# Performance work log

Hardware: AMD Instinct MI355X
Metric: run time of the kernel (lower is better)

## Reference

```python
import jax, jax.numpy as jnp
import numpy as np

INPUT_SIZE = 128
HIDDEN_SIZE = 128
BATCH = 65536
K = INPUT_SIZE + HIDDEN_SIZE


def setup_inputs() -> dict:
    key = jax.random.key(0)
    ks = jax.random.split(key, 11)
    bound = 1.0 / np.sqrt(K)  # nn.Linear default init range
    inp = {
        "input": jax.random.normal(ks[0], (BATCH, INPUT_SIZE), dtype=jnp.float32),
        "hidden": jax.random.normal(ks[1], (BATCH, HIDDEN_SIZE), dtype=jnp.float32),
        "cell": jax.random.normal(ks[2], (BATCH, HIDDEN_SIZE), dtype=jnp.float32),
        # Four gate linears: weights [hidden, K], biases [hidden]
        "W_f": jax.random.uniform(ks[3], (HIDDEN_SIZE, K), jnp.float32, -bound, bound),
        "b_f": jax.random.uniform(ks[4], (HIDDEN_SIZE,), jnp.float32, -bound, bound),
        "W_i": jax.random.uniform(ks[5], (HIDDEN_SIZE, K), jnp.float32, -bound, bound),
        "b_i": jax.random.uniform(ks[6], (HIDDEN_SIZE,), jnp.float32, -bound, bound),
        "W_o": jax.random.uniform(ks[7], (HIDDEN_SIZE, K), jnp.float32, -bound, bound),
        "b_o": jax.random.uniform(ks[8], (HIDDEN_SIZE,), jnp.float32, -bound, bound),
        "W_c": jax.random.uniform(ks[9], (HIDDEN_SIZE, K), jnp.float32, -bound, bound),
        "b_c": jax.random.uniform(ks[10], (HIDDEN_SIZE,), jnp.float32, -bound, bound),
    }
    return inp


def reference(input, hidden, cell, W_f, b_f, W_i, b_i, W_o, b_o, W_c, b_c):
    # combined = cat([input, hidden], axis=1); fuse 4 gate GEMMs into one
    combined = jnp.concatenate([input, hidden], axis=1)  # [B, K]
    W = jnp.concatenate([W_f, W_i, W_o, W_c], axis=0)    # [4H, K]
    b = jnp.concatenate([b_f, b_i, b_o, b_c], axis=0)    # [4H]
    gates = combined @ W.T + b                            # [B, 4H]
    f, i, o, g = jnp.split(gates, 4, axis=1)
    forget_gate = jax.nn.sigmoid(f)
    input_gate = jax.nn.sigmoid(i)
    output_gate = jax.nn.sigmoid(o)
    cell_gate = jnp.tanh(g)
    new_cell = forget_gate * cell + input_gate * cell_gate
    new_hidden = output_gate * jnp.tanh(new_cell)
    return (new_hidden, new_cell)
```

## Files before the change

kernel.cpp:

```cpp
#include <hip/hip_runtime.h>
#include <hip/hip_bf16.h>

#define BATCH   65536
#define FEAT    128
#define KDIM    256

typedef __attribute__((ext_vector_type(8))) short bf16x8;
typedef __attribute__((ext_vector_type(4))) float f32x4;

__device__ __forceinline__ short f2bf(float f) {
    return __builtin_bit_cast(short, __float2bfloat16(f));
}

__device__ __forceinline__ bf16x8 cvt8(f32x4 lo, f32x4 hi) {
    bf16x8 r;
    r[0] = f2bf(lo[0]); r[1] = f2bf(lo[1]); r[2] = f2bf(lo[2]); r[3] = f2bf(lo[3]);
    r[4] = f2bf(hi[0]); r[5] = f2bf(hi[1]); r[6] = f2bf(hi[2]); r[7] = f2bf(hi[3]);
    return r;
}

__device__ __forceinline__ float sigmoidf_(float x) {
    return 1.0f / (1.0f + __expf(-x));
}
__device__ __forceinline__ float tanhf_(float x) {
    float xc = fminf(fmaxf(x, -15.0f), 15.0f);
    float e = __expf(-2.0f * xc);
    return (1.0f - e) / (1.0f + e);
}

__global__ __launch_bounds__(256, 4)
void lstm_ksplit(const float* __restrict__ inp, const float* __restrict__ hid,
                 const float* __restrict__ cel,
                 const float* __restrict__ Wf, const float* __restrict__ bfp,
                 const float* __restrict__ Wi, const float* __restrict__ bip,
                 const float* __restrict__ Wo, const float* __restrict__ bop,
                 const float* __restrict__ Wc, const float* __restrict__ bcp,
                 float* __restrict__ out)
{
    __shared__ float lds[4][64][35];

    const int tid  = threadIdx.x;
    const int lane = tid & 63;
    const int wid  = tid >> 6;
    const int bid  = blockIdx.x;
    const int cg   = bid >> 7;
    const int rtg  = bid & 127;

    const int lr = lane & 15;
    const int lk = lane >> 4;
    const int j  = cg * 16 + lr;

    const int kq = wid;
    const int k0 = (kq & 1) * 64;
    const float* Asrc = (kq < 2) ? inp : hid;

    bf16x8 w[4][2];
    {
        const float* wsrc[4] = {Wf, Wi, Wo, Wc};
        #pragma unroll
        for (int g = 0; g < 4; ++g) {
            const float* s = wsrc[g] + (size_t)j * KDIM + kq * 64 + lk * 8;
            #pragma unroll
            for (int ks = 0; ks < 2; ++ks) {
                f32x4 lo = *(const f32x4*)(s + ks * 32);
                f32x4 hi = *(const f32x4*)(s + ks * 32 + 4);
                w[g][ks] = cvt8(lo, hi);
            }
        }
    }
    const float bsf = bfp[j], bsi = bip[j], bso = bop[j], bsc = bcp[j];

    float* outH = out;
    float* outC = out + (size_t)BATCH * FEAT;

    for (int it = 0; it < 16; ++it) {
        const int R0 = (rtg + it * 128) * 32;

        const float* a = Asrc + (size_t)(R0 + lr) * FEAT + k0 + lk * 8;
        f32x4 alo[2][2], ahi[2][2];
        #pragma unroll
        for (int ks = 0; ks < 2; ++ks)
            #pragma unroll
            for (int mb = 0; mb < 2; ++mb) {
                alo[ks][mb] = *(const f32x4*)(a + mb * 16 * FEAT + ks * 32);
                ahi[ks][mb] = *(const f32x4*)(a + mb * 16 * FEAT + ks * 32 + 4);
            }

        f32x4 acc[2][4];
        #pragma unroll
        for (int mb = 0; mb < 2; ++mb)
            #pragma unroll
            for (int g = 0; g < 4; ++g)
                acc[mb][g] = (f32x4){0.f, 0.f, 0.f, 0.f};

        #pragma unroll
        for (int ks = 0; ks < 2; ++ks) {
            bf16x8 a0 = cvt8(alo[ks][0], ahi[ks][0]);
            bf16x8 a1 = cvt8(alo[ks][1], ahi[ks][1]);
            #pragma unroll
            for (int g = 0; g < 4; ++g) {
                acc[0][g] = __builtin_amdgcn_mfma_f32_16x16x32_bf16(a0, w[g][ks], acc[0][g], 0, 0, 0);
                acc[1][g] = __builtin_amdgcn_mfma_f32_16x16x32_bf16(a1, w[g][ks], acc[1][g], 0, 0, 0);
            }
        }

        #pragma unroll
        for (int mb = 0; mb < 2; ++mb)
            #pragma unroll
            for (int g = 0; g < 4; ++g)
                #pragma unroll
                for (int t = 0; t < 4; ++t)
                    lds[kq][lane][mb * 16 + g * 4 + t] = acc[mb][g][t];
        __syncthreads();

        #pragma unroll
        for (int p = 0; p < 2; ++p) {
            const int rl  = wid * 8 + p * 4 + (lane >> 4);
            const int jc  = lane & 15;
            const int mb  = rl >> 4;
            const int lk2 = (rl >> 2) & 3;
            const int t   = rl & 3;
            const int sl  = lk2 * 16 + jc;

            float s0 = 0.f, s1 = 0.f, s2 = 0.f, s3 = 0.f;
            #pragma unroll
            for (int q = 0; q < 4; ++q) {
                s0 += lds[q][sl][mb * 16 + 0 * 4 + t];
                s1 += lds[q][sl][mb * 16 + 1 * 4 + t];
                s2 += lds[q][sl][mb * 16 + 2 * 4 + t];
                s3 += lds[q][sl][mb * 16 + 3 * 4 + t];
            }

            const int R = R0 + rl;
            const size_t off = (size_t)R * FEAT + cg * 16 + jc;
            float cv = cel[off];
            float fg = sigmoidf_(s0 + bsf);
            float ig = sigmoidf_(s1 + bsi);
            float og = sigmoidf_(s2 + bso);
            float gg = tanhf_(s3 + bsc);
            float nc = fg * cv + ig * gg;
            float nh = og * tanhf_(nc);
            outH[off] = nh;
            outC[off] = nc;
        }
        __syncthreads();
    }
}

extern "C" void kernel_launch(void* const* d_in, const int* in_sizes, int n_in,
                              void* d_out, int out_size, void* d_ws, size_t ws_size,
                              hipStream_t stream) {
    const float* inp = (const float*)d_in[0];
    const float* hid = (const float*)d_in[1];
    const float* cel = (const float*)d_in[2];
    const float* Wf  = (const float*)d_in[3];
    const float* bf  = (const float*)d_in[4];
    const float* Wi  = (const float*)d_in[5];
    const float* bi  = (const float*)d_in[6];
    const float* Wo  = (const float*)d_in[7];
    const float* bo  = (const float*)d_in[8];
    const float* Wc  = (const float*)d_in[9];
    const float* bc  = (const float*)d_in[10];
    float* out = (float*)d_out;

    lstm_ksplit<<<dim3(1024), dim3(256), 0, stream>>>(
        inp, hid, cel, Wf, bf, Wi, bi, Wo, bo, Wc, bc, out);
}
```

Before: 213.5 us.

## Prefetch next tile's activations and cell, double-buffer packed bf16 partial sums

Loads the next iteration's A-operand rows and cell values into registers before the current tile's reduction and epilogue, so global-load latency overlaps with compute. The LDS partial-sum buffer is double-buffered, which removes the second barrier per iteration. Partial sums are packed as bf16 pairs, halving LDS traffic and footprint. This lowers precision of the k-split reduction and raises register pressure.

```diff
diff --git a/kernel.cpp b/kernel.cpp
--- a/kernel.cpp
+++ b/kernel.cpp
@@ -19,6 +19,18 @@
     return r;
 }
 
+__device__ __forceinline__ unsigned int pk2(float a, float b) {
+    unsigned short ua = __builtin_bit_cast(unsigned short, __float2bfloat16(a));
+    unsigned short ub = __builtin_bit_cast(unsigned short, __float2bfloat16(b));
+    return (unsigned int)ua | ((unsigned int)ub << 16);
+}
+__device__ __forceinline__ float bflo(unsigned int p) {
+    return __builtin_bit_cast(float, p << 16);
+}
+__device__ __forceinline__ float bfhi(unsigned int p) {
+    return __builtin_bit_cast(float, p & 0xffff0000u);
+}
+
 __device__ __forceinline__ float sigmoidf_(float x) {
     return 1.0f / (1.0f + __expf(-x));
 }
@@ -29,15 +41,15 @@
 }
 
 __global__ __launch_bounds__(256, 4)
-void lstm_ksplit(const float* __restrict__ inp, const float* __restrict__ hid,
-                 const float* __restrict__ cel,
-                 const float* __restrict__ Wf, const float* __restrict__ bfp,
-                 const float* __restrict__ Wi, const float* __restrict__ bip,
-                 const float* __restrict__ Wo, const float* __restrict__ bop,
-                 const float* __restrict__ Wc, const float* __restrict__ bcp,
-                 float* __restrict__ out)
+void lstm_v3(const float* __restrict__ inp, const float* __restrict__ hid,
+             const float* __restrict__ cel,
+             const float* __restrict__ Wf, const float* __restrict__ bfp,
+             const float* __restrict__ Wi, const float* __restrict__ bip,
+             const float* __restrict__ Wo, const float* __restrict__ bop,
+             const float* __restrict__ Wc, const float* __restrict__ bcp,
+             float* __restrict__ out)
 {
-    __shared__ float lds[4][64][35];
+    __shared__ unsigned int plds[2][4][64][17];
 
     const int tid  = threadIdx.x;
     const int lane = tid & 63;
@@ -73,11 +85,9 @@
     float* outH = out;
     float* outC = out + (size_t)BATCH * FEAT;
 
-    for (int it = 0; it < 16; ++it) {
-        const int R0 = (rtg + it * 128) * 32;
-
-        const float* a = Asrc + (size_t)(R0 + lr) * FEAT + k0 + lk * 8;
-        f32x4 alo[2][2], ahi[2][2];
+    f32x4 alo[2][2], ahi[2][2];
+    {
+        const float* a = Asrc + (size_t)((rtg * 32) + lr) * FEAT + k0 + lk * 8;
         #pragma unroll
         for (int ks = 0; ks < 2; ++ks)
             #pragma unroll
@@ -85,6 +95,16 @@
                 alo[ks][mb] = *(const f32x4*)(a + mb * 16 * FEAT + ks * 32);
                 ahi[ks][mb] = *(const f32x4*)(a + mb * 16 * FEAT + ks * 32 + 4);
             }
+    }
+    float cv[2];
+    #pragma unroll
+    for (int p = 0; p < 2; ++p) {
+        const int rl = wid * 8 + p * 4 + lk;
+        cv[p] = cel[(size_t)(rtg * 32 + rl) * FEAT + j];
+    }
+
+    for (int it = 0; it < 16; ++it) {
+        const int R0 = (rtg + it * 128) * 32;
 
         f32x4 acc[2][4];
         #pragma unroll
@@ -104,19 +124,34 @@
             }
         }
 
-        #pragma unroll
-        for (int mb = 0; mb < 2; ++mb)
-            #pragma unroll
-            for (int g = 0; g < 4; ++g)
+        if (it < 15) {
+            const int R0n = (rtg + (it + 1) * 128) * 32;
+            const float* an = Asrc + (size_t)(R0n + lr) * FEAT + k0 + lk * 8;
+            #pragma unroll
+            for (int ks = 0; ks < 2; ++ks)
                 #pragma unroll
-                for (int t = 0; t < 4; ++t)
-                    lds[kq][lane][mb * 16 + g * 4 + t] = acc[mb][g][t];
+                for (int mb = 0; mb < 2; ++mb) {
+                    alo[ks][mb] = *(const f32x4*)(an + mb * 16 * FEAT + ks * 32);
+                    ahi[ks][mb] = *(const f32x4*)(an + mb * 16 * FEAT + ks * 32 + 4);
+                }
+        }
+
+        {
+            unsigned int* dst = &plds[it & 1][kq][lane][0];
+            #pragma unroll
+            for (int mb = 0; mb < 2; ++mb)
+                #pragma unroll
+                for (int t = 0; t < 4; ++t) {
+                    dst[mb * 8 + t * 2 + 0] = pk2(acc[mb][0][t], acc[mb][1][t]);
+                    dst[mb * 8 + t * 2 + 1] = pk2(acc[mb][2][t], acc[mb][3][t]);
+                }
+        }
         __syncthreads();
 
         #pragma unroll
         for (int p = 0; p < 2; ++p) {
-            const int rl  = wid * 8 + p * 4 + (lane >> 4);
-            const int jc  = lane & 15;
+            const int rl  = wid * 8 + p * 4 + lk;
+            const int jc  = lr;
             const int mb  = rl >> 4;
             const int lk2 = (rl >> 2) & 3;
             const int t   = rl & 3;
@@ -125,25 +160,31 @@
             float s0 = 0.f, s1 = 0.f, s2 = 0.f, s3 = 0.f;
             #pragma unroll
             for (int q = 0; q < 4; ++q) {
-                s0 += lds[q][sl][mb * 16 + 0 * 4 + t];
-                s1 += lds[q][sl][mb * 16 + 1 * 4 + t];
-                s2 += lds[q][sl][mb * 16 + 2 * 4 + t];
-                s3 += lds[q][sl][mb * 16 + 3 * 4 + t];
-            }
-
-            const int R = R0 + rl;
-            const size_t off = (size_t)R * FEAT + cg * 16 + jc;
-            float cv = cel[off];
+                unsigned int pA = plds[it & 1][q][sl][mb * 8 + t * 2 + 0];
+                unsigned int pB = plds[it & 1][q][sl][mb * 8 + t * 2 + 1];
+                s0 += bflo(pA); s1 += bfhi(pA);
+                s2 += bflo(pB); s3 += bfhi(pB);
+            }
+
+            const size_t off = (size_t)(R0 + rl) * FEAT + j;
             float fg = sigmoidf_(s0 + bsf);
             float ig = sigmoidf_(s1 + bsi);
             float og = sigmoidf_(s2 + bso);
             float gg = tanhf_(s3 + bsc);
-            float nc = fg * cv + ig * gg;
+            float nc = fg * cv[p] + ig * gg;
             float nh = og * tanhf_(nc);
             outH[off] = nh;
             outC[off] = nc;
         }
-        __syncthreads();
+
+        if (it < 15) {
+            const int R0n = (rtg + (it + 1) * 128) * 32;
+            #pragma unroll
+            for (int p = 0; p < 2; ++p) {
+                const int rl = wid * 8 + p * 4 + lk;
+                cv[p] = cel[(size_t)(R0n + rl) * FEAT + j];
+            }
+        }
     }
 }
 
@@ -163,6 +204,6 @@
     const float* bc  = (const float*)d_in[10];
     float* out = (float*)d_out;
 
-    lstm_ksplit<<<dim3(1024), dim3(256), 0, stream>>>(
+    lstm_v3<<<dim3(1024), dim3(256), 0, stream>>>(
         inp, hid, cel, Wf, bf, Wi, bi, Wo, bo, Wc, bc, out);
 }
```

New measurement: 219.8 us. 3.0% more time.
